# Kernel tuning notes

Measured on AMD Instinct MI355X. Metric: run time of the kernel, lower is better.

The kernel has to match this reference:

```python
import jax, jax.numpy as jnp
import numpy as np

NUM_CAPSULES = 16
IN_DIM = 512
OUT_DIM = 32
ROUTING_ITERS = 3
EPS = 1e-08


def setup_inputs() -> dict:
    key = jax.random.key(0)
    kx, kw = jax.random.split(key)
    x = jax.random.normal(kx, (32768, IN_DIM), dtype=jnp.float32)
    W = jax.random.normal(kw, (IN_DIM, NUM_CAPSULES * OUT_DIM), dtype=jnp.float32)
    return {"x": x, "W": W}


def squash(s):
    # s: [batch, out_dim]
    norm = jnp.sum(s * s, axis=-1, keepdims=True)
    scale = norm / (1.0 + norm)
    return scale * s / (jnp.sqrt(norm) + EPS)


def reference(x, W):
    batch = x.shape[0]
    # u: [batch, num_capsules, out_dim]
    u = jnp.matmul(x, W).reshape(batch, NUM_CAPSULES, OUT_DIM)
    b = jnp.zeros((batch, NUM_CAPSULES), dtype=x.dtype)
    v = None
    for _ in range(ROUTING_ITERS):
        c = jax.nn.softmax(b, axis=1)[..., None]       # [batch, caps, 1]
        s = jnp.sum(c * u, axis=1)                      # [batch, out_dim]
        v = squash(s)                                   # [batch, out_dim]
        b = b + jnp.sum(u * v[:, None, :], axis=-1)     # [batch, caps]
    return v
```

## Files before the change

### kernel.cpp

```cpp
#include <hip/hip_runtime.h>
#include <math.h>


#define BATCH   32768
#define KDIM    512
#define NDIM    512
#define OUT_DIM 32
#define EPS_F   1e-8f
#define NKT     32

typedef _Float16 half8  __attribute__((ext_vector_type(8)));
typedef float   floatx4 __attribute__((ext_vector_type(4)));
typedef float  floatx16 __attribute__((ext_vector_type(16)));

__global__ void prep_w(const float* __restrict__ W, _Float16* __restrict__ Wh,
                       _Float16* __restrict__ Wl) {
    __shared__ float tile[32][33];
    const int tx = threadIdx.x, ty = threadIdx.y;
    const int n0 = blockIdx.x * 32, k0 = blockIdx.y * 32;
#pragma unroll
    for (int i = 0; i < 4; ++i)
        tile[ty + 8 * i][tx] = W[(size_t)(k0 + ty + 8 * i) * NDIM + n0 + tx];
    __syncthreads();
#pragma unroll
    for (int i = 0; i < 4; ++i) {
        const int k = k0 + tx, n = n0 + ty + 8 * i;
        const float v = tile[tx][ty + 8 * i];
        const _Float16 h = (_Float16)v;
        const _Float16 l = (_Float16)(v - (float)h);
        const size_t off = (size_t)(k >> 4) * (NDIM * 16) + (size_t)n * 16 + (k & 15);
        Wh[off] = h;
        Wl[off] = l;
    }
}

__device__ __forceinline__ void ld_g2l_16(void* lds_base_uniform, const void* g) {
    __builtin_amdgcn_global_load_lds(
        (const __attribute__((address_space(1))) void*)g,
        (__attribute__((address_space(3))) void*)lds_base_uniform, 16, 0, 0);
}

__global__ __launch_bounds__(512, 4)
void capsule_mfma(const float* __restrict__ x, const _Float16* __restrict__ Wh,
                  const _Float16* __restrict__ Wl, float* __restrict__ out) {
    __shared__ __align__(16) char smem[66560];
    _Float16 (*Bs)[2][NDIM][16] = (_Float16 (*)[2][NDIM][16])smem;
    float (*u_lds)[520] = (float (*)[520])smem;

    const int tid  = threadIdx.x;
    const int w    = tid >> 6;
    const int lane = tid & 63;
    const int r = w >> 2, c = w & 3;
    const int ln = lane & 31, q = lane >> 5;
    const int rowBlk = blockIdx.x * 64;
    const int R0 = rowBlk + r * 32;
    const int C0 = c * 128;

    floatx16 acc[4];
#pragma unroll
    for (int nt = 0; nt < 4; ++nt)
#pragma unroll
        for (int i = 0; i < 16; ++i) acc[nt][i] = 0.f;

    const float* aptr = x + (size_t)(R0 + ln) * KDIM + q * 8;

    const int nseg = w * 64;

    {
        const size_t g0 = 0;
        ld_g2l_16(&Bs[0][0][nseg][0],      Wh + g0 + (size_t)nseg * 16 + lane * 8);
        ld_g2l_16(&Bs[0][0][nseg + 32][0], Wh + g0 + (size_t)(nseg + 32) * 16 + lane * 8);
        ld_g2l_16(&Bs[0][1][nseg][0],      Wl + g0 + (size_t)nseg * 16 + lane * 8);
        ld_g2l_16(&Bs[0][1][nseg + 32][0], Wl + g0 + (size_t)(nseg + 32) * 16 + lane * 8);
    }
    floatx4 a0 = *(const floatx4*)(aptr);
    floatx4 a1 = *(const floatx4*)(aptr + 4);

#pragma unroll 2
    for (int kt = 0; kt < NKT; ++kt) {
        __syncthreads();
        const int buf = kt & 1;
        if (kt + 1 < NKT) {
            const size_t g = (size_t)(kt + 1) * (NDIM * 16);
            ld_g2l_16(&Bs[buf ^ 1][0][nseg][0],      Wh + g + (size_t)nseg * 16 + lane * 8);
            ld_g2l_16(&Bs[buf ^ 1][0][nseg + 32][0], Wh + g + (size_t)(nseg + 32) * 16 + lane * 8);
            ld_g2l_16(&Bs[buf ^ 1][1][nseg][0],      Wl + g + (size_t)nseg * 16 + lane * 8);
            ld_g2l_16(&Bs[buf ^ 1][1][nseg + 32][0], Wl + g + (size_t)(nseg + 32) * 16 + lane * 8);
        }
        floatx4 p0, p1;
        if (kt + 1 < NKT) {
            p0 = *(const floatx4*)(aptr + (kt + 1) * 16);
            p1 = *(const floatx4*)(aptr + (kt + 1) * 16 + 4);
        }
        const float av[8] = {a0[0], a0[1], a0[2], a0[3], a1[0], a1[1], a1[2], a1[3]};
        half8 ah, al;
#pragma unroll
        for (int j = 0; j < 8; ++j) {
            const _Float16 h = (_Float16)av[j];
            ah[j] = h;
            al[j] = (_Float16)(av[j] - (float)h);
        }
#pragma unroll
        for (int nt = 0; nt < 4; ++nt) {
            const half8 bh = *(const half8*)&Bs[buf][0][C0 + nt * 32 + ln][q * 8];
            const half8 bl = *(const half8*)&Bs[buf][1][C0 + nt * 32 + ln][q * 8];
            acc[nt] = __builtin_amdgcn_mfma_f32_32x32x16_f16(ah, bh, acc[nt], 0, 0, 0);
            acc[nt] = __builtin_amdgcn_mfma_f32_32x32x16_f16(al, bh, acc[nt], 0, 0, 0);
            acc[nt] = __builtin_amdgcn_mfma_f32_32x32x16_f16(ah, bl, acc[nt], 0, 0, 0);
        }
        if (kt + 1 < NKT) { a0 = p0; a1 = p1; }
    }

    const int dgrp = lane & 3;
    for (int p = 0; p < 2; ++p) {
        __syncthreads();
        if (r == p) {
#pragma unroll
            for (int nt = 0; nt < 4; ++nt)
#pragma unroll
                for (int reg = 0; reg < 16; ++reg)
                    u_lds[(reg & 3) + 8 * (reg >> 2) + 4 * q][C0 + nt * 32 + ln] = acc[nt][reg];
        }
        __syncthreads();
#pragma unroll 1
        for (int ri = 0; ri < 4; ++ri) {
            const int rl = w * 4 + ri;
            const floatx4 ua = *(const floatx4*)&u_lds[rl][lane * 8];
            const floatx4 ub = *(const floatx4*)&u_lds[rl][lane * 8 + 4];
            const float u8[8] = {ua[0], ua[1], ua[2], ua[3],
                                 ub[0], ub[1], ub[2], ub[3]};
            float b_own = 0.f;
            float v[8];
#pragma unroll
            for (int it = 0; it < 3; ++it) {
                float c_own;
                if (it == 0) {
                    c_own = 1.0f / 16.0f;
                } else {
                    float m = b_own;
#pragma unroll
                    for (int mask = 4; mask <= 32; mask <<= 1)
                        m = fmaxf(m, __shfl_xor(m, mask));
                    const float e = __expf(b_own - m);
                    float ssum = e;
#pragma unroll
                    for (int mask = 4; mask <= 32; mask <<= 1)
                        ssum += __shfl_xor(ssum, mask);
                    c_own = e / ssum;
                }
                float s[8];
#pragma unroll
                for (int j = 0; j < 8; ++j) s[j] = c_own * u8[j];
#pragma unroll
                for (int mask = 4; mask <= 32; mask <<= 1) {
#pragma unroll
                    for (int j = 0; j < 8; ++j) s[j] += __shfl_xor(s[j], mask);
                }
                float nrm = 0.f;
#pragma unroll
                for (int j = 0; j < 8; ++j) nrm = fmaf(s[j], s[j], nrm);
                nrm += __shfl_xor(nrm, 1);
                nrm += __shfl_xor(nrm, 2);
                const float scale = nrm / ((1.f + nrm) * (sqrtf(nrm) + EPS_F));
#pragma unroll
                for (int j = 0; j < 8; ++j) v[j] = scale * s[j];
                if (it < 2) {
                    float dot = 0.f;
#pragma unroll
                    for (int j = 0; j < 8; ++j) dot = fmaf(u8[j], v[j], dot);
                    dot += __shfl_xor(dot, 1);
                    dot += __shfl_xor(dot, 2);
                    b_own += dot;
                }
            }
            if (lane < 4) {
                float4* o = (float4*)(out + (size_t)(rowBlk + p * 32 + rl) * OUT_DIM
                                      + dgrp * 8);
                o[0] = make_float4(v[0], v[1], v[2], v[3]);
                o[1] = make_float4(v[4], v[5], v[6], v[7]);
            }
        }
    }
}

extern "C" void kernel_launch(void* const* d_in, const int* in_sizes, int n_in,
                              void* d_out, int out_size, void* d_ws, size_t ws_size,
                              hipStream_t stream) {
    const float* x = (const float*)d_in[0];
    const float* W = (const float*)d_in[1];
    float* out = (float*)d_out;
    _Float16* Wh = (_Float16*)d_ws;
    _Float16* Wl = Wh + (size_t)NDIM * KDIM;

    prep_w<<<dim3(16, 16), dim3(32, 8), 0, stream>>>(W, Wh, Wl);
    capsule_mfma<<<dim3(BATCH / 64), dim3(512), 0, stream>>>(x, Wh, Wl, out);
}
```

Before: 183.0 us.

## Double rows per block for B-tile reuse and use DPP cross-lane reductions

Each block now covers 128 rows instead of 64, and each wave computes two 32-row MFMA fragments. This reuses every LDS-loaded W tile across twice as many rows and halves W global traffic per row. Separately, the routing reductions replace ds_bpermute-based __shfl_xor with DPP row-rotate and ds_swizzle moves. The cost is double the accumulator registers (launch bounds lowered to 2 blocks) and half as many blocks, which lowers occupancy.

Result: slower. 446.9 us (+144.2%).

```diff
diff --git a/kernel.cpp b/kernel.cpp
--- a/kernel.cpp
+++ b/kernel.cpp
@@ -12,6 +12,39 @@
 typedef _Float16 half8  __attribute__((ext_vector_type(8)));
 typedef float   floatx4 __attribute__((ext_vector_type(4)));
 typedef float  floatx16 __attribute__((ext_vector_type(16)));
+
+template <int CTRL>
+__device__ __forceinline__ float dpp_mov(float x) {
+    return __int_as_float(__builtin_amdgcn_mov_dpp(__float_as_int(x), CTRL, 0xF, 0xF, true));
+}
+template <int XMASK>
+__device__ __forceinline__ float swz_xor(float x) {
+    return __int_as_float(__builtin_amdgcn_ds_swizzle(__float_as_int(x), (XMASK << 10) | 31));
+}
+#define ROR4  0x124
+#define ROR8  0x128
+#define QXOR1 0xB1
+#define QXOR2 0x4E
+
+__device__ __forceinline__ float cap_sum(float x) {
+    x += dpp_mov<ROR4>(x);
+    x += dpp_mov<ROR8>(x);
+    x += swz_xor<16>(x);
+    x += __shfl_xor(x, 32);
+    return x;
+}
+__device__ __forceinline__ float cap_max(float x) {
+    x = fmaxf(x, dpp_mov<ROR4>(x));
+    x = fmaxf(x, dpp_mov<ROR8>(x));
+    x = fmaxf(x, swz_xor<16>(x));
+    x = fmaxf(x, __shfl_xor(x, 32));
+    return x;
+}
+__device__ __forceinline__ float dg_sum(float x) {
+    x += dpp_mov<QXOR1>(x);
+    x += dpp_mov<QXOR2>(x);
+    return x;
+}
 
 __global__ void prep_w(const float* __restrict__ W, _Float16* __restrict__ Wh,
                        _Float16* __restrict__ Wl) {
@@ -40,7 +73,7 @@
         (__attribute__((address_space(3))) void*)lds_base_uniform, 16, 0, 0);
 }
 
-__global__ __launch_bounds__(512, 4)
+__global__ __launch_bounds__(512, 2)
 void capsule_mfma(const float* __restrict__ x, const _Float16* __restrict__ Wh,
                   const _Float16* __restrict__ Wl, float* __restrict__ out) {
     __shared__ __align__(16) char smem[66560];
@@ -52,29 +85,32 @@
     const int lane = tid & 63;
     const int r = w >> 2, c = w & 3;
     const int ln = lane & 31, q = lane >> 5;
-    const int rowBlk = blockIdx.x * 64;
-    const int R0 = rowBlk + r * 32;
+    const int rowBlk = blockIdx.x * 128;
+    const int R0 = rowBlk + r * 64;
     const int C0 = c * 128;
 
-    floatx16 acc[4];
-#pragma unroll
-    for (int nt = 0; nt < 4; ++nt)
-#pragma unroll
-        for (int i = 0; i < 16; ++i) acc[nt][i] = 0.f;
-
-    const float* aptr = x + (size_t)(R0 + ln) * KDIM + q * 8;
+    floatx16 acc[2][4];
+#pragma unroll
+    for (int mf = 0; mf < 2; ++mf)
+#pragma unroll
+        for (int nt = 0; nt < 4; ++nt)
+#pragma unroll
+            for (int i = 0; i < 16; ++i) acc[mf][nt][i] = 0.f;
+
+    const float* aptr0 = x + (size_t)(R0 + ln) * KDIM + q * 8;
+    const float* aptr1 = aptr0 + (size_t)32 * KDIM;
 
     const int nseg = w * 64;
 
-    {
-        const size_t g0 = 0;
-        ld_g2l_16(&Bs[0][0][nseg][0],      Wh + g0 + (size_t)nseg * 16 + lane * 8);
-        ld_g2l_16(&Bs[0][0][nseg + 32][0], Wh + g0 + (size_t)(nseg + 32) * 16 + lane * 8);
-        ld_g2l_16(&Bs[0][1][nseg][0],      Wl + g0 + (size_t)nseg * 16 + lane * 8);
-        ld_g2l_16(&Bs[0][1][nseg + 32][0], Wl + g0 + (size_t)(nseg + 32) * 16 + lane * 8);
-    }
-    floatx4 a0 = *(const floatx4*)(aptr);
-    floatx4 a1 = *(const floatx4*)(aptr + 4);
+    ld_g2l_16(&Bs[0][0][nseg][0],      Wh + (size_t)nseg * 16 + lane * 8);
+    ld_g2l_16(&Bs[0][0][nseg + 32][0], Wh + (size_t)(nseg + 32) * 16 + lane * 8);
+    ld_g2l_16(&Bs[0][1][nseg][0],      Wl + (size_t)nseg * 16 + lane * 8);
+    ld_g2l_16(&Bs[0][1][nseg + 32][0], Wl + (size_t)(nseg + 32) * 16 + lane * 8);
+    floatx4 a[2][2];
+    a[0][0] = *(const floatx4*)(aptr0);
+    a[0][1] = *(const floatx4*)(aptr0 + 4);
+    a[1][0] = *(const floatx4*)(aptr1);
+    a[1][1] = *(const floatx4*)(aptr1 + 4);
 
 #pragma unroll 2
     for (int kt = 0; kt < NKT; ++kt) {
@@ -87,39 +123,52 @@
             ld_g2l_16(&Bs[buf ^ 1][1][nseg][0],      Wl + g + (size_t)nseg * 16 + lane * 8);
             ld_g2l_16(&Bs[buf ^ 1][1][nseg + 32][0], Wl + g + (size_t)(nseg + 32) * 16 + lane * 8);
         }
-        floatx4 p0, p1;
+        floatx4 pr[2][2];
         if (kt + 1 < NKT) {
-            p0 = *(const floatx4*)(aptr + (kt + 1) * 16);
-            p1 = *(const floatx4*)(aptr + (kt + 1) * 16 + 4);
-        }
-        const float av[8] = {a0[0], a0[1], a0[2], a0[3], a1[0], a1[1], a1[2], a1[3]};
-        half8 ah, al;
-#pragma unroll
-        for (int j = 0; j < 8; ++j) {
-            const _Float16 h = (_Float16)av[j];
-            ah[j] = h;
-            al[j] = (_Float16)(av[j] - (float)h);
+            pr[0][0] = *(const floatx4*)(aptr0 + (kt + 1) * 16);
+            pr[0][1] = *(const floatx4*)(aptr0 + (kt + 1) * 16 + 4);
+            pr[1][0] = *(const floatx4*)(aptr1 + (kt + 1) * 16);
+            pr[1][1] = *(const floatx4*)(aptr1 + (kt + 1) * 16 + 4);
+        }
+        half8 ah[2], al[2];
+#pragma unroll
+        for (int mf = 0; mf < 2; ++mf) {
+            const float av[8] = {a[mf][0][0], a[mf][0][1], a[mf][0][2], a[mf][0][3],
+                                 a[mf][1][0], a[mf][1][1], a[mf][1][2], a[mf][1][3]};
+#pragma unroll
+            for (int j = 0; j < 8; ++j) {
+                const _Float16 h = (_Float16)av[j];
+                ah[mf][j] = h;
+                al[mf][j] = (_Float16)(av[j] - (float)h);
+            }
         }
 #pragma unroll
         for (int nt = 0; nt < 4; ++nt) {
             const half8 bh = *(const half8*)&Bs[buf][0][C0 + nt * 32 + ln][q * 8];
             const half8 bl = *(const half8*)&Bs[buf][1][C0 + nt * 32 + ln][q * 8];
-            acc[nt] = __builtin_amdgcn_mfma_f32_32x32x16_f16(ah, bh, acc[nt], 0, 0, 0);
-            acc[nt] = __builtin_amdgcn_mfma_f32_32x32x16_f16(al, bh, acc[nt], 0, 0, 0);
-            acc[nt] = __builtin_amdgcn_mfma_f32_32x32x16_f16(ah, bl, acc[nt], 0, 0, 0);
-        }
-        if (kt + 1 < NKT) { a0 = p0; a1 = p1; }
+#pragma unroll
+            for (int mf = 0; mf < 2; ++mf) {
+                acc[mf][nt] = __builtin_amdgcn_mfma_f32_32x32x16_f16(ah[mf], bh, acc[mf][nt], 0, 0, 0);
+                acc[mf][nt] = __builtin_amdgcn_mfma_f32_32x32x16_f16(al[mf], bh, acc[mf][nt], 0, 0, 0);
+                acc[mf][nt] = __builtin_amdgcn_mfma_f32_32x32x16_f16(ah[mf], bl, acc[mf][nt], 0, 0, 0);
+            }
+        }
+        if (kt + 1 < NKT) {
+#pragma unroll
+            for (int mf = 0; mf < 2; ++mf) { a[mf][0] = pr[mf][0]; a[mf][1] = pr[mf][1]; }
+        }
     }
 
     const int dgrp = lane & 3;
-    for (int p = 0; p < 2; ++p) {
+    for (int p = 0; p < 4; ++p) {
         __syncthreads();
-        if (r == p) {
+        if (r == (p >> 1)) {
+            const int mf = p & 1;
 #pragma unroll
             for (int nt = 0; nt < 4; ++nt)
 #pragma unroll
                 for (int reg = 0; reg < 16; ++reg)
-                    u_lds[(reg & 3) + 8 * (reg >> 2) + 4 * q][C0 + nt * 32 + ln] = acc[nt][reg];
+                    u_lds[(reg & 3) + 8 * (reg >> 2) + 4 * q][C0 + nt * 32 + ln] = acc[mf][nt][reg];
         }
         __syncthreads();
 #pragma unroll 1
@@ -137,30 +186,26 @@
                 if (it == 0) {
                     c_own = 1.0f / 16.0f;
                 } else {
-                    float m = b_own;
-#pragma unroll
-                    for (int mask = 4; mask <= 32; mask <<= 1)
-                        m = fmaxf(m, __shfl_xor(m, mask));
+                    const float m = cap_max(b_own);
                     const float e = __expf(b_own - m);
-                    float ssum = e;
-#pragma unroll
-                    for (int mask = 4; mask <= 32; mask <<= 1)
-                        ssum += __shfl_xor(ssum, mask);
+                    const float ssum = cap_sum(e);
                     c_own = e / ssum;
                 }
                 float s[8];
 #pragma unroll
                 for (int j = 0; j < 8; ++j) s[j] = c_own * u8[j];
 #pragma unroll
-                for (int mask = 4; mask <= 32; mask <<= 1) {
-#pragma unroll
-                    for (int j = 0; j < 8; ++j) s[j] += __shfl_xor(s[j], mask);
-                }
+                for (int j = 0; j < 8; ++j) s[j] += dpp_mov<ROR4>(s[j]);
+#pragma unroll
+                for (int j = 0; j < 8; ++j) s[j] += dpp_mov<ROR8>(s[j]);
+#pragma unroll
+                for (int j = 0; j < 8; ++j) s[j] += swz_xor<16>(s[j]);
+#pragma unroll
+                for (int j = 0; j < 8; ++j) s[j] += __shfl_xor(s[j], 32);
                 float nrm = 0.f;
 #pragma unroll
                 for (int j = 0; j < 8; ++j) nrm = fmaf(s[j], s[j], nrm);
-                nrm += __shfl_xor(nrm, 1);
-                nrm += __shfl_xor(nrm, 2);
+                nrm = dg_sum(nrm);
                 const float scale = nrm / ((1.f + nrm) * (sqrtf(nrm) + EPS_F));
 #pragma unroll
                 for (int j = 0; j < 8; ++j) v[j] = scale * s[j];
@@ -168,8 +213,7 @@
                     float dot = 0.f;
 #pragma unroll
                     for (int j = 0; j < 8; ++j) dot = fmaf(u8[j], v[j], dot);
-                    dot += __shfl_xor(dot, 1);
-                    dot += __shfl_xor(dot, 2);
+                    dot = dg_sum(dot);
                     b_own += dot;
                 }
             }
@@ -193,5 +237,5 @@
     _Float16* Wl = Wh + (size_t)NDIM * KDIM;
 
     prep_w<<<dim3(16, 16), dim3(32, 8), 0, stream>>>(W, Wh, Wl);
-    capsule_mfma<<<dim3(BATCH / 64), dim3(512), 0, stream>>>(x, Wh, Wl, out);
-}
+    capsule_mfma<<<dim3(BATCH / 128), dim3(512), 0, stream>>>(x, Wh, Wl, out);
+}
```
